# Kernel optimization log

Hardware: AMD Instinct MI355X
Metric: run time of the kernel (lower is better)

## Reference

```python
import jax, jax.numpy as jnp
import numpy as np

N_NODES = 50000
N_EDGES = 800000
IN_C = 16
HID_C = 16
OUT_C = 10
N_GRAPHS = 500
EDGE_DIM = 3
MLP_HID = 25
BN_EPS = 1e-5


def setup_inputs() -> dict:
    key = jax.random.key(0)
    ks = iter(jax.random.split(key, 40))

    def nrm(shape, scale=1.0):
        return jax.random.normal(next(ks), shape, dtype=jnp.float32) * scale

    inp = {}
    inp["x"] = nrm((N_NODES, IN_C))
    inp["edge_index"] = jax.random.randint(next(ks), (2, N_EDGES), 0, N_NODES, dtype=jnp.int32)
    inp["edge_attr"] = jax.random.uniform(next(ks), (N_EDGES, EDGE_DIM), dtype=jnp.float32)
    inp["batch"] = jnp.sort(jax.random.randint(next(ks), (N_NODES,), 0, N_GRAPHS, dtype=jnp.int32))

    def bn_params():
        g = jax.random.uniform(next(ks), (MLP_HID,), minval=0.8, maxval=1.2, dtype=jnp.float32)
        b = nrm((MLP_HID,), 0.1)
        mu = nrm((MLP_HID,), 0.1)
        var = jax.random.uniform(next(ks), (MLP_HID,), minval=0.5, maxval=1.5, dtype=jnp.float32)
        return g, b, mu, var

    # edge MLP 1: 3 -> 25 -> IN_C*HID_C
    inp["W1a"] = nrm((EDGE_DIM, MLP_HID), 0.3)
    inp["b1a"] = nrm((MLP_HID,), 0.05)
    inp["g1"], inp["bt1"], inp["m1"], inp["v1"] = bn_params()
    inp["W1b"] = nrm((MLP_HID, IN_C * HID_C), 0.1)
    inp["b1b"] = nrm((IN_C * HID_C,), 0.05)
    inp["root1"] = nrm((IN_C, HID_C), 0.2)
    inp["bias1"] = nrm((HID_C,), 0.05)

    # edge MLP 2: 3 -> 25 -> HID_C*HID_C
    inp["W2a"] = nrm((EDGE_DIM, MLP_HID), 0.3)
    inp["b2a"] = nrm((MLP_HID,), 0.05)
    inp["g2"], inp["bt2"], inp["m2"], inp["v2"] = bn_params()
    inp["W2b"] = nrm((MLP_HID, HID_C * HID_C), 0.1)
    inp["b2b"] = nrm((HID_C * HID_C,), 0.05)
    inp["root2"] = nrm((HID_C, HID_C), 0.2)
    inp["bias2"] = nrm((HID_C,), 0.05)

    # final MLP([HID_C, OUT_C]) -> single plain linear (plain_last)
    inp["fcW"] = nrm((HID_C, OUT_C), 0.2)
    inp["fcb"] = nrm((OUT_C,), 0.05)
    return inp


def _edge_mlp(e, Wa, ba, g, bt, mu, var, Wb, bb):
    # Linear -> BatchNorm(eval) -> ReLU -> (dropout=eval identity) -> Linear
    h = e @ Wa + ba
    h = g * (h - mu) * jax.lax.rsqrt(var + BN_EPS) + bt
    h = jax.nn.relu(h)
    return h @ Wb + bb


def _nnconv(x, src, dst, w_edge, root, bias, out_dim):
    # message: x_j [E,in] times per-edge weight [E,in,out]
    msg = jnp.einsum("ei,eio->eo", x[src], w_edge)
    agg = jax.ops.segment_sum(msg, dst, num_segments=N_NODES)
    deg = jax.ops.segment_sum(jnp.ones((src.shape[0],), msg.dtype), dst, num_segments=N_NODES)
    agg = agg / jnp.maximum(deg, 1.0)[:, None]  # mean aggregation
    return agg + x @ root + bias


def reference(x, edge_index, edge_attr, batch,
              W1a, b1a, g1, bt1, m1, v1, W1b, b1b, root1, bias1,
              W2a, b2a, g2, bt2, m2, v2, W2b, b2b, root2, bias2,
              fcW, fcb):
    src, dst = edge_index[0], edge_index[1]

    w1 = _edge_mlp(edge_attr, W1a, b1a, g1, bt1, m1, v1, W1b, b1b).reshape(-1, IN_C, HID_C)
    x = jax.nn.elu(_nnconv(x, src, dst, w1, root1, bias1, HID_C))

    w2 = _edge_mlp(edge_attr, W2a, b2a, g2, bt2, m2, v2, W2b, b2b).reshape(-1, HID_C, HID_C)
    x = jax.nn.elu(_nnconv(x, src, dst, w2, root2, bias2, HID_C))

    # global mean pooling over graphs
    pooled = jax.ops.segment_sum(x, batch, num_segments=N_GRAPHS)
    cnt = jax.ops.segment_sum(jnp.ones((x.shape[0],), x.dtype), batch, num_segments=N_GRAPHS)
    pooled = pooled / jnp.maximum(cnt, 1.0)[:, None]

    return pooled @ fcW + fcb  # [N_GRAPHS, OUT_C]
```

## Files before the change

### kernel.cpp

```cpp
#include <hip/hip_runtime.h>
#include <math.h>

#define N_NODES 50000
#define N_EDGES 800000
#define IN_C 16
#define HID_C 16
#define OUT_C 10
#define N_GRAPHS 500
#define EDGE_DIM 3
#define MLP_HID 25
#define BN_EPS 1e-5f

#define SCAN_NB ((N_NODES + 255) / 256)

typedef __attribute__((ext_vector_type(8))) _Float16 half8;
typedef __attribute__((ext_vector_type(2))) _Float16 half2v;
typedef __attribute__((ext_vector_type(4))) float f32x4;
union U4H8 { uint4 u; half8 h; half2v p[4]; };
union HU { _Float16 h; unsigned short u; };


__global__ __launch_bounds__(256) void setup_kernel(
    const float* __restrict__ W1a, const float* __restrict__ b1a,
    const float* __restrict__ g1, const float* __restrict__ bt1,
    const float* __restrict__ m1, const float* __restrict__ v1,
    const float* __restrict__ W2a, const float* __restrict__ b2a,
    const float* __restrict__ g2, const float* __restrict__ bt2,
    const float* __restrict__ m2, const float* __restrict__ v2,
    const float* __restrict__ W1b, const float* __restrict__ b1b,
    const float* __restrict__ W2b, const float* __restrict__ b2b,
    const int* __restrict__ batch,
    float* __restrict__ AC1, float* __restrict__ AC2,
    unsigned int* __restrict__ WF1, unsigned int* __restrict__ WF2,
    int* __restrict__ goff, int* __restrict__ cnt, int* __restrict__ ticket)
{
    const int blk = blockIdx.x;
    const int tid = threadIdx.x;
    if (blk < 7) {
        int t = blk * 256 + tid;
        if (t >= 1664) return;
        const float *Wb, *bb; unsigned int *WH;
        int tl = t;
        if (t < 832) { Wb = W1b; bb = b1b; WH = WF1; }
        else { tl = t - 832; Wb = W2b; bb = b2b; WH = WF2; }
        int m = tl >> 6;
        int L = tl & 63;
        int q = L >> 4, o = L & 15;
        unsigned int hi[8];
        for (int j = 0; j < 8; ++j) {
            int kp = m*32 + q*8 + j;
            int k = kp >> 4, i = kp & 15;
            float w = (k < 25) ? Wb[k*256 + i*16 + o] : bb[i*16 + o];
            HU cv; cv.h = (_Float16)w;
            hi[j] = cv.u;
        }
        int base = (m*64 + L) * 4;
        for (int d = 0; d < 4; ++d)
            WH[base + d] = hi[2*d] | (hi[2*d+1] << 16);
        return;
    }
    if (blk == 7 || blk == 8) {
        if (blk == 7) {
            if (tid < 26) {
                int k = tid;
                if (k < 25) {
                    float sc = g1[k] / sqrtf(v1[k] + BN_EPS);
                    AC1[k*4+0] = sc * W1a[0*MLP_HID+k];
                    AC1[k*4+1] = sc * W1a[1*MLP_HID+k];
                    AC1[k*4+2] = sc * W1a[2*MLP_HID+k];
                    AC1[k*4+3] = sc * (b1a[k] - m1[k]) + bt1[k];
                } else {
                    AC1[100] = 0.f; AC1[101] = 0.f; AC1[102] = 0.f; AC1[103] = 1.f;
                }
            } else if (tid >= 32 && tid < 58) {
                int k = tid - 32;
                if (k < 25) {
                    float sc = g2[k] / sqrtf(v2[k] + BN_EPS);
                    AC2[k*4+0] = sc * W2a[0*MLP_HID+k];
                    AC2[k*4+1] = sc * W2a[1*MLP_HID+k];
                    AC2[k*4+2] = sc * W2a[2*MLP_HID+k];
                    AC2[k*4+3] = sc * (b2a[k] - m2[k]) + bt2[k];
                } else {
                    AC2[100] = 0.f; AC2[101] = 0.f; AC2[102] = 0.f; AC2[103] = 1.f;
                }
            }
        }
        int g = (blk - 7) * 256 + tid;
        if (g <= N_GRAPHS) {
            int lo = 0, hi = N_NODES;
            while (lo < hi) {
                int mid = (lo + hi) >> 1;
                if (batch[mid] < g) lo = mid + 1; else hi = mid;
            }
            goff[g] = lo;
        }
        return;
    }
    int idx = (blk - 9) * 256 + tid;
    if (idx < N_NODES) cnt[idx] = 0;
    if (blk == 9 && tid == 0) *ticket = 0;
}


__global__ __launch_bounds__(256) void rank_kernel(const int* __restrict__ dst,
                                                   int* __restrict__ cnt,
                                                   int* __restrict__ rank) {
    int e = blockIdx.x * blockDim.x + threadIdx.x;
    if (e < N_EDGES) rank[e] = atomicAdd(&cnt[dst[e]], 1);
}

__global__ __launch_bounds__(256) void scan_p1(const int* __restrict__ cnt,
                                               int* __restrict__ bsum,
                                               int* __restrict__ bpre,
                                               int* __restrict__ off,
                                               int* __restrict__ ticket) {
    __shared__ int lds[256];
    __shared__ int sDone;
    int t = threadIdx.x;
    int idx = blockIdx.x * 256 + t;
    lds[t] = (idx < N_NODES) ? cnt[idx] : 0;
    __syncthreads();
    for (int d = 128; d > 0; d >>= 1) {
        if (t < d) lds[t] += lds[t + d];
        __syncthreads();
    }
    if (t == 0) {
        bsum[blockIdx.x] = lds[0];
        __threadfence();
        sDone = atomicAdd(ticket, 1);
    }
    __syncthreads();
    if (sDone != SCAN_NB - 1) return;
    __threadfence();
    int v = (t < SCAN_NB) ? bsum[t] : 0;
    __syncthreads();
    lds[t] = v;
    __syncthreads();
    for (int d = 1; d < 256; d <<= 1) {
        int u = (t >= d) ? lds[t - d] : 0;
        __syncthreads();
        lds[t] += u;
        __syncthreads();
    }
    if (t < SCAN_NB) bpre[t] = (t > 0) ? lds[t - 1] : 0;
    if (t == 255) off[N_NODES] = lds[255];
}

__global__ __launch_bounds__(256) void scan_p3(const int* __restrict__ cnt,
                                               const int* __restrict__ bpre,
                                               int* __restrict__ off) {
    __shared__ int lds[256];
    int t = threadIdx.x;
    int idx = blockIdx.x * 256 + t;
    int v = (idx < N_NODES) ? cnt[idx] : 0;
    lds[t] = v;
    __syncthreads();
    for (int d = 1; d < 256; d <<= 1) {
        int u = (t >= d) ? lds[t - d] : 0;
        __syncthreads();
        lds[t] += u;
        __syncthreads();
    }
    if (idx < N_NODES) off[idx] = bpre[blockIdx.x] + lds[t] - v;
}


__global__ __launch_bounds__(256) void edge_mfma5_kernel(
    const float* __restrict__ xin,
    const int* __restrict__ src,
    const int* __restrict__ dst,
    const int* __restrict__ rank,
    const int* __restrict__ off,
    const float* __restrict__ eattr,
    const float* __restrict__ AC,
    const unsigned int* __restrict__ WF,
    float* __restrict__ msg_buf)
{
    const int tid  = threadIdx.x;
    const int wave = tid >> 6;
    const int lane = tid & 63;
    const int q    = lane >> 4;
    const int el   = lane & 15;
    const int i0   = (q & 1) * 8;
    const bool bsel = (q >> 1) != 0;
    const int E0   = (blockIdx.x * 4 + wave) * 32;
    const int eA   = E0 + el;
    const int eB   = E0 + 16 + el;

    const int sA = src[eA], sB = src[eB];
    const int pA = off[dst[eA]] + rank[eA];
    const int pB = off[dst[eB]] + rank[eB];
    const float aA0 = eattr[(size_t)eA*3+0];
    const float aA1 = eattr[(size_t)eA*3+1];
    const float aA2 = eattr[(size_t)eA*3+2];
    const float aB0 = eattr[(size_t)eB*3+0];
    const float aB1 = eattr[(size_t)eB*3+1];
    const float aB2 = eattr[(size_t)eB*3+2];
    const float4* xpA = (const float4*)(xin + (size_t)sA*16 + i0);
    const float4 xlA = xpA[0], xhA = xpA[1];
    const float4* xpB = (const float4*)(xin + (size_t)sB*16 + i0);
    const float4 xlB = xpB[0], xhB = xpB[1];

    U4H8 xA, xB;
    {
        const float x8A[8] = {xlA.x,xlA.y,xlA.z,xlA.w,xhA.x,xhA.y,xhA.z,xhA.w};
        const float x8B[8] = {xlB.x,xlB.y,xlB.z,xlB.w,xhB.x,xhB.y,xhB.z,xhB.w};
        #pragma unroll
        for (int j = 0; j < 4; ++j) {
            half2v ta; ta.x = (_Float16)x8A[2*j]; ta.y = (_Float16)x8A[2*j+1];
            half2v tb; tb.x = (_Float16)x8B[2*j]; tb.y = (_Float16)x8B[2*j+1];
            xA.p[j] = ta; xB.p[j] = tb;
        }
    }

    f32x4 accA = {0.f, 0.f, 0.f, 0.f};
    f32x4 accB = {0.f, 0.f, 0.f, 0.f};
    #pragma unroll 1
    for (int m = 0; m < 13; ++m) {
        const float4 Ae = *(const float4*)(AC + m*8);
        const float4 Ao = *(const float4*)(AC + m*8 + 4);
        const float A0 = bsel ? Ao.x : Ae.x;
        const float A1 = bsel ? Ao.y : Ae.y;
        const float A2 = bsel ? Ao.z : Ae.z;
        const float A3 = bsel ? Ao.w : Ae.w;
        U4H8 w; w.u = ((const uint4*)WF)[m*64 + lane];
        float hA = fmaxf(fmaf(aA2, A2, fmaf(aA1, A1, fmaf(aA0, A0, A3))), 0.f);
        float hB = fmaxf(fmaf(aB2, A2, fmaf(aB1, A1, fmaf(aB0, A0, A3))), 0.f);
        _Float16 ha = (_Float16)hA, hb = (_Float16)hB;
        half2v hA2; hA2.x = ha; hA2.y = ha;
        half2v hB2; hB2.x = hb; hB2.y = hb;
        U4H8 fA, fB;
        #pragma unroll
        for (int j = 0; j < 4; ++j) {
            fA.p[j] = hA2 * xA.p[j];
            fB.p[j] = hB2 * xB.p[j];
        }
        accA = __builtin_amdgcn_mfma_f32_16x16x32_f16(fA.h, w.h, accA, 0, 0, 0);
        accB = __builtin_amdgcn_mfma_f32_16x16x32_f16(fB.h, w.h, accB, 0, 0, 0);
    }

    #pragma unroll
    for (int r = 0; r < 4; ++r) {
        int rowA = __shfl(pA, q*4 + r);
        int rowB = __shfl(pB, q*4 + r);
        msg_buf[(size_t)rowA * HID_C + el] = accA[r];
        msg_buf[(size_t)rowB * HID_C + el] = accB[r];
    }
}

__global__ __launch_bounds__(256) void node_gather_kernel(
    const float* __restrict__ xin, const float* __restrict__ msg_buf,
    const int* __restrict__ off,
    const float* __restrict__ root, const float* __restrict__ bias,
    float* __restrict__ xout)
{
    int t = blockIdx.x * blockDim.x + threadIdx.x;
    int n = t >> 4;
    int o = t & 15;
    if (n >= N_NODES) return;
    int lo = off[n], hi = off[n+1];
    float inv = 1.f / fmaxf((float)(hi - lo), 1.f);

    float s0 = 0.f, s1 = 0.f, s2 = 0.f, s3 = 0.f;
    int r = lo;
    for (; r + 4 <= hi; r += 4) {
        s0 += msg_buf[(size_t)r     * HID_C + o];
        s1 += msg_buf[(size_t)(r+1) * HID_C + o];
        s2 += msg_buf[(size_t)(r+2) * HID_C + o];
        s3 += msg_buf[(size_t)(r+3) * HID_C + o];
    }
    for (; r < hi; ++r) s0 += msg_buf[(size_t)r * HID_C + o];
    float s = (s0 + s1) + (s2 + s3);

    float acc = fmaf(s, inv, bias[o]);
    const float* xr = xin + (size_t)n * IN_C;
    #pragma unroll
    for (int i = 0; i < IN_C; ++i)
        acc = fmaf(xr[i], root[i*HID_C+o], acc);
    xout[(size_t)n*HID_C + o] = acc > 0.f ? acc : (expf(acc) - 1.f);
}

__global__ __launch_bounds__(64) void pool_final_kernel(
    const float* __restrict__ xin, const int* __restrict__ goff,
    const float* __restrict__ fcW, const float* __restrict__ fcb,
    float* __restrict__ out)
{
    __shared__ float part[4][HID_C];
    __shared__ float pooled[HID_C];
    int g = blockIdx.x;
    int t = threadIdx.x;
    int c = t & 15, sub = t >> 4;
    int lo = goff[g], hi = goff[g+1];
    float s = 0.f;
    for (int n = lo + sub; n < hi; n += 4)
        s += xin[(size_t)n*HID_C + c];
    part[sub][c] = s;
    __syncthreads();
    if (t < HID_C) {
        pooled[t] = (part[0][t] + part[1][t] + part[2][t] + part[3][t])
                    / fmaxf((float)(hi - lo), 1.f);
    }
    __syncthreads();
    if (t < OUT_C) {
        float acc = fcb[t];
        #pragma unroll
        for (int i = 0; i < HID_C; ++i)
            acc = fmaf(pooled[i], fcW[i*OUT_C+t], acc);
        out[g*OUT_C + t] = acc;
    }
}


extern "C" void kernel_launch(void* const* d_in, const int* in_sizes, int n_in,
                              void* d_out, int out_size, void* d_ws, size_t ws_size,
                              hipStream_t stream)
{
    const float* x     = (const float*)d_in[0];
    const int*   ei    = (const int*)d_in[1];
    const float* eattr = (const float*)d_in[2];
    const int*   batch = (const int*)d_in[3];
    const float* W1a   = (const float*)d_in[4];
    const float* b1a   = (const float*)d_in[5];
    const float* g1    = (const float*)d_in[6];
    const float* bt1   = (const float*)d_in[7];
    const float* m1    = (const float*)d_in[8];
    const float* v1    = (const float*)d_in[9];
    const float* W1b   = (const float*)d_in[10];
    const float* b1b   = (const float*)d_in[11];
    const float* root1 = (const float*)d_in[12];
    const float* bias1 = (const float*)d_in[13];
    const float* W2a   = (const float*)d_in[14];
    const float* b2a   = (const float*)d_in[15];
    const float* g2    = (const float*)d_in[16];
    const float* bt2   = (const float*)d_in[17];
    const float* m2    = (const float*)d_in[18];
    const float* v2    = (const float*)d_in[19];
    const float* W2b   = (const float*)d_in[20];
    const float* b2b   = (const float*)d_in[21];
    const float* root2 = (const float*)d_in[22];
    const float* bias2 = (const float*)d_in[23];
    const float* fcW   = (const float*)d_in[24];
    const float* fcb   = (const float*)d_in[25];

    const int* src = ei;
    const int* dst = ei + N_EDGES;

    float* ws   = (float*)d_ws;
    float* MSG  = ws;
    float* X1   = ws + 12800000;
    float* X2   = ws + 13600000;
    int*   RANK = (int*)(ws + 14400000);
    int*   CNT  = (int*)(ws + 15200000);
    int*   OFF  = (int*)(ws + 15250000);
    int*   GOFF = (int*)(ws + 15300064);
    unsigned int* WF1 = (unsigned int*)(ws + 15300576);
    unsigned int* WF2 = (unsigned int*)(ws + 15303904);
    float* AC1  = ws + 15307232;
    float* AC2  = ws + 15307344;
    int*   BSUM = (int*)(ws + 15307456);
    int*   BPRE = (int*)(ws + 15307712);
    int*   TICK = (int*)(ws + 15307968);

    setup_kernel<<<9 + SCAN_NB, 256, 0, stream>>>(
        W1a, b1a, g1, bt1, m1, v1, W2a, b2a, g2, bt2, m2, v2,
        W1b, b1b, W2b, b2b, batch, AC1, AC2, WF1, WF2, GOFF, CNT, TICK);
    rank_kernel<<<N_EDGES/256, 256, 0, stream>>>(dst, CNT, RANK);
    scan_p1<<<SCAN_NB, 256, 0, stream>>>(CNT, BSUM, BPRE, OFF, TICK);
    scan_p3<<<SCAN_NB, 256, 0, stream>>>(CNT, BPRE, OFF);

    edge_mfma5_kernel<<<N_EDGES/128, 256, 0, stream>>>(x, src, dst, RANK, OFF,
                                                       eattr, AC1, WF1, MSG);
    node_gather_kernel<<<(N_NODES*16+255)/256, 256, 0, stream>>>(x, MSG, OFF,
                                                                 root1, bias1, X1);

    edge_mfma5_kernel<<<N_EDGES/128, 256, 0, stream>>>(X1, src, dst, RANK, OFF,
                                                       eattr, AC2, WF2, MSG);
    node_gather_kernel<<<(N_NODES*16+255)/256, 256, 0, stream>>>(X1, MSG, OFF,
                                                                 root2, bias2, X2);

    pool_final_kernel<<<N_GRAPHS, 64, 0, stream>>>(X2, GOFF, fcW, fcb, (float*)d_out);
}
```

Before: 269.7 us.

## Process 64 edges per wave with LDS-staged weights and swapped MFMA operands

The edge kernel now gives each wave 64 edges (four MFMA tiles) instead of 32. The 13x64 fp16 weight fragments are staged once per block in shared memory rather than read from global memory on every loop iteration. The MFMA operands are swapped so that each lane holds four consecutive output channels of one edge, which allows a single 16-byte vector store per tile into the message buffer instead of scalar scattered stores. This halves the grid and raises per-thread register use; it also adds a block-level barrier and 13 KB of LDS per block, which may reduce occupancy.

```diff
diff --git a/kernel.cpp b/kernel.cpp
--- a/kernel.cpp
+++ b/kernel.cpp
@@ -165,7 +165,7 @@
 }
 
 
-__global__ __launch_bounds__(256) void edge_mfma5_kernel(
+__global__ __launch_bounds__(256) void edge_mfma6_kernel(
     const float* __restrict__ xin,
     const int* __restrict__ src,
     const int* __restrict__ dst,
@@ -176,45 +176,54 @@
     const unsigned int* __restrict__ WF,
     float* __restrict__ msg_buf)
 {
-    const int tid  = threadIdx.x;
+    __shared__ uint4 wf_s[832];
+    const int tid = threadIdx.x;
+    #pragma unroll
+    for (int it = 0; it < 4; ++it) {
+        int gi = tid + it*256;
+        if (gi < 832) wf_s[gi] = ((const uint4*)WF)[gi];
+    }
+    __syncthreads();
+
     const int wave = tid >> 6;
     const int lane = tid & 63;
     const int q    = lane >> 4;
     const int el   = lane & 15;
     const int i0   = (q & 1) * 8;
     const bool bsel = (q >> 1) != 0;
-    const int E0   = (blockIdx.x * 4 + wave) * 32;
-    const int eA   = E0 + el;
-    const int eB   = E0 + 16 + el;
-
-    const int sA = src[eA], sB = src[eB];
-    const int pA = off[dst[eA]] + rank[eA];
-    const int pB = off[dst[eB]] + rank[eB];
-    const float aA0 = eattr[(size_t)eA*3+0];
-    const float aA1 = eattr[(size_t)eA*3+1];
-    const float aA2 = eattr[(size_t)eA*3+2];
-    const float aB0 = eattr[(size_t)eB*3+0];
-    const float aB1 = eattr[(size_t)eB*3+1];
-    const float aB2 = eattr[(size_t)eB*3+2];
-    const float4* xpA = (const float4*)(xin + (size_t)sA*16 + i0);
-    const float4 xlA = xpA[0], xhA = xpA[1];
-    const float4* xpB = (const float4*)(xin + (size_t)sB*16 + i0);
-    const float4 xlB = xpB[0], xhB = xpB[1];
-
-    U4H8 xA, xB;
-    {
-        const float x8A[8] = {xlA.x,xlA.y,xlA.z,xlA.w,xhA.x,xhA.y,xhA.z,xhA.w};
-        const float x8B[8] = {xlB.x,xlB.y,xlB.z,xlB.w,xhB.x,xhB.y,xhB.z,xhB.w};
+    const int E0   = (blockIdx.x * 4 + wave) * 64;
+
+    const int sAll = src[E0 + lane];
+    const int dAll = dst[E0 + lane];
+    const int rAll = rank[E0 + lane];
+    const int pAll = off[dAll] + rAll;
+
+    int   sT[4];
+    float a0[4], a1[4], a2[4];
+    #pragma unroll
+    for (int t = 0; t < 4; ++t) {
+        sT[t] = __shfl(sAll, t*16 + el);
+        int e = E0 + t*16 + el;
+        a0[t] = eattr[(size_t)e*3+0];
+        a1[t] = eattr[(size_t)e*3+1];
+        a2[t] = eattr[(size_t)e*3+2];
+    }
+
+    U4H8 xf[4];
+    #pragma unroll
+    for (int t = 0; t < 4; ++t) {
+        const float4* xp = (const float4*)(xin + (size_t)sT[t]*16 + i0);
+        const float4 xl = xp[0], xh = xp[1];
+        const float x8[8] = {xl.x,xl.y,xl.z,xl.w,xh.x,xh.y,xh.z,xh.w};
         #pragma unroll
         for (int j = 0; j < 4; ++j) {
-            half2v ta; ta.x = (_Float16)x8A[2*j]; ta.y = (_Float16)x8A[2*j+1];
-            half2v tb; tb.x = (_Float16)x8B[2*j]; tb.y = (_Float16)x8B[2*j+1];
-            xA.p[j] = ta; xB.p[j] = tb;
-        }
-    }
-
-    f32x4 accA = {0.f, 0.f, 0.f, 0.f};
-    f32x4 accB = {0.f, 0.f, 0.f, 0.f};
+            half2v tv; tv.x = (_Float16)x8[2*j]; tv.y = (_Float16)x8[2*j+1];
+            xf[t].p[j] = tv;
+        }
+    }
+
+    f32x4 acc0 = {0.f,0.f,0.f,0.f}, acc1 = {0.f,0.f,0.f,0.f};
+    f32x4 acc2 = {0.f,0.f,0.f,0.f}, acc3 = {0.f,0.f,0.f,0.f};
     #pragma unroll 1
     for (int m = 0; m < 13; ++m) {
         const float4 Ae = *(const float4*)(AC + m*8);
@@ -223,28 +232,28 @@
         const float A1 = bsel ? Ao.y : Ae.y;
         const float A2 = bsel ? Ao.z : Ae.z;
         const float A3 = bsel ? Ao.w : Ae.w;
-        U4H8 w; w.u = ((const uint4*)WF)[m*64 + lane];
-        float hA = fmaxf(fmaf(aA2, A2, fmaf(aA1, A1, fmaf(aA0, A0, A3))), 0.f);
-        float hB = fmaxf(fmaf(aB2, A2, fmaf(aB1, A1, fmaf(aB0, A0, A3))), 0.f);
-        _Float16 ha = (_Float16)hA, hb = (_Float16)hB;
-        half2v hA2; hA2.x = ha; hA2.y = ha;
-        half2v hB2; hB2.x = hb; hB2.y = hb;
-        U4H8 fA, fB;
+        U4H8 w; w.u = wf_s[m*64 + lane];
         #pragma unroll
-        for (int j = 0; j < 4; ++j) {
-            fA.p[j] = hA2 * xA.p[j];
-            fB.p[j] = hB2 * xB.p[j];
-        }
-        accA = __builtin_amdgcn_mfma_f32_16x16x32_f16(fA.h, w.h, accA, 0, 0, 0);
-        accB = __builtin_amdgcn_mfma_f32_16x16x32_f16(fB.h, w.h, accB, 0, 0, 0);
-    }
-
-    #pragma unroll
-    for (int r = 0; r < 4; ++r) {
-        int rowA = __shfl(pA, q*4 + r);
-        int rowB = __shfl(pB, q*4 + r);
-        msg_buf[(size_t)rowA * HID_C + el] = accA[r];
-        msg_buf[(size_t)rowB * HID_C + el] = accB[r];
+        for (int t = 0; t < 4; ++t) {
+            float h = fmaxf(fmaf(a2[t], A2, fmaf(a1[t], A1,
+                              fmaf(a0[t], A0, A3))), 0.f);
+            _Float16 hh = (_Float16)h;
+            half2v h2; h2.x = hh; h2.y = hh;
+            U4H8 f;
+            #pragma unroll
+            for (int j = 0; j < 4; ++j) f.p[j] = h2 * xf[t].p[j];
+            f32x4 a = (t==0) ? acc0 : (t==1) ? acc1 : (t==2) ? acc2 : acc3;
+            a = __builtin_amdgcn_mfma_f32_16x16x32_f16(w.h, f.h, a, 0, 0, 0);
+            if (t==0) acc0 = a; else if (t==1) acc1 = a;
+            else if (t==2) acc2 = a; else acc3 = a;
+        }
+    }
+
+    #pragma unroll
+    for (int t = 0; t < 4; ++t) {
+        int row = __shfl(pAll, t*16 + el);
+        f32x4 a = (t==0) ? acc0 : (t==1) ? acc1 : (t==2) ? acc2 : acc3;
+        *(f32x4*)(msg_buf + (size_t)row * HID_C + q*4) = a;
     }
 }
 
@@ -368,12 +377,12 @@
     scan_p1<<<SCAN_NB, 256, 0, stream>>>(CNT, BSUM, BPRE, OFF, TICK);
     scan_p3<<<SCAN_NB, 256, 0, stream>>>(CNT, BPRE, OFF);
 
-    edge_mfma5_kernel<<<N_EDGES/128, 256, 0, stream>>>(x, src, dst, RANK, OFF,
+    edge_mfma6_kernel<<<N_EDGES/256, 256, 0, stream>>>(x, src, dst, RANK, OFF,
                                                        eattr, AC1, WF1, MSG);
     node_gather_kernel<<<(N_NODES*16+255)/256, 256, 0, stream>>>(x, MSG, OFF,
                                                                  root1, bias1, X1);
 
-    edge_mfma5_kernel<<<N_EDGES/128, 256, 0, stream>>>(X1, src, dst, RANK, OFF,
+    edge_mfma6_kernel<<<N_EDGES/256, 256, 0, stream>>>(X1, src, dst, RANK, OFF,
                                                        eattr, AC2, WF2, MSG);
     node_gather_kernel<<<(N_NODES*16+255)/256, 256, 0, stream>>>(X1, MSG, OFF,
                                                                  root2, bias2, X2);
```

New measurement: 260.5 us. 1.04x faster.
